# Optimization experiments

Hardware: AMD Instinct MI355X
Metric: run time of the kernel (lower is better)

The kernel has to match this reference:

```python
import jax, jax.numpy as jnp
import numpy as np

N = 5
RANK = 3
IMW = IMH = 1024
S = IMW * IMH
RANKLIST = [1] + [RANK] * (N - 1) + [1]  # [1,3,3,3,3,1]


def _xavier_std(shape):
    # torch xavier_normal_ on a 3D tensor (a, b, c): fan_in = b*c, fan_out = a*c
    a, b, c = shape
    fan_in, fan_out = b * c, a * c
    return float(np.sqrt(2.0 / (fan_in + fan_out)))


def setup_inputs() -> dict:
    key = jax.random.key(0)
    keys = jax.random.split(key, N + 1)
    inp = {"z": jax.random.normal(keys[0], (S,), dtype=jnp.float32)}
    for n in range(N):
        shp = (RANKLIST[n], S, RANKLIST[n + 1])
        inp[f"TT{n}"] = jax.random.normal(keys[n + 1], shp, dtype=jnp.float32) * _xavier_std(shp)
    return inp


def reference(z, TT0, TT1, TT2, TT3, TT4):
    # V[k] = z @ TT[k] : contract the s axis -> (r_k, r_{k+1}); tiny matrices.
    f = jnp.einsum('s,rsq->rq', z, TT0)          # (1, 3)
    for core in (TT1, TT2, TT3):
        f = f @ jnp.einsum('s,rsq->rq', z, core)  # (1, 3)
    # Last factor: the slice TT[N-1][:, :, 0] itself (NOT contracted with z).
    f = f @ TT4[:, :, 0]                          # (1, s)
    return f.reshape(-1)                          # (s,)
```

## Files before the change

kernel.cpp:

```cpp
#include <hip/hip_runtime.h>

#define SDIM (1024 * 1024)
#define GROUPS (SDIM / 4)
#define K1_BLOCKS 1024
#define K1_THREADS 256
#define NACC 30
#define PART_STRIDE 32

__device__ __forceinline__ float wave_reduce(float v) {
    #pragma unroll
    for (int off = 32; off > 0; off >>= 1)
        v += __shfl_down(v, off, 64);
    return v;
}

__global__ __launch_bounds__(K1_THREADS) void ftt_k1(
    const float* __restrict__ z,
    const float* __restrict__ t0,
    const float* __restrict__ t1,
    const float* __restrict__ t2,
    const float* __restrict__ t3,
    float* __restrict__ partials)
{
    float acc[NACC];
    #pragma unroll
    for (int i = 0; i < NACC; ++i) acc[i] = 0.0f;

    const int g = blockIdx.x * K1_THREADS + threadIdx.x;

    const float4 z4 = reinterpret_cast<const float4*>(z)[g];
    const float zz[4] = {z4.x, z4.y, z4.z, z4.w};

    {
        const float4* p = reinterpret_cast<const float4*>(t0 + 12 * g);
        const float4 c0 = p[0], c1 = p[1], c2 = p[2];
        const float tt[12] = {c0.x, c0.y, c0.z, c0.w,
                              c1.x, c1.y, c1.z, c1.w,
                              c2.x, c2.y, c2.z, c2.w};
        #pragma unroll
        for (int j = 0; j < 4; ++j)
            #pragma unroll
            for (int q = 0; q < 3; ++q)
                acc[q] += zz[j] * tt[j * 3 + q];
    }

    const float* __restrict__ Ts[3] = {t1, t2, t3};
    #pragma unroll
    for (int k = 0; k < 3; ++k) {
        #pragma unroll
        for (int r = 0; r < 3; ++r) {
            const float4* p = reinterpret_cast<const float4*>(Ts[k] + r * 3 * SDIM + 12 * g);
            const float4 c0 = p[0], c1 = p[1], c2 = p[2];
            const float tt[12] = {c0.x, c0.y, c0.z, c0.w,
                                  c1.x, c1.y, c1.z, c1.w,
                                  c2.x, c2.y, c2.z, c2.w};
            #pragma unroll
            for (int j = 0; j < 4; ++j)
                #pragma unroll
                for (int q = 0; q < 3; ++q)
                    acc[3 + k * 9 + r * 3 + q] += zz[j] * tt[j * 3 + q];
        }
    }

    #pragma unroll
    for (int i = 0; i < NACC; ++i)
        acc[i] = wave_reduce(acc[i]);

    __shared__ float red[4][NACC];
    const int lane = threadIdx.x & 63;
    const int wave = threadIdx.x >> 6;
    if (lane == 0) {
        #pragma unroll
        for (int i = 0; i < NACC; ++i) red[wave][i] = acc[i];
    }
    __syncthreads();
    if (threadIdx.x < NACC) {
        const float s = red[0][threadIdx.x] + red[1][threadIdx.x] +
                        red[2][threadIdx.x] + red[3][threadIdx.x];
        partials[blockIdx.x * PART_STRIDE + threadIdx.x] = s;
    }
}

__global__ __launch_bounds__(256) void ftt_k2(
    const float* __restrict__ partials,
    float* __restrict__ fvec)
{
    __shared__ float part[8][32];
    const int c = threadIdx.x & 31;
    const int grp = threadIdx.x >> 5;
    float s = 0.0f;
    const int b0 = grp * (K1_BLOCKS / 8);
    for (int b = b0; b < b0 + (K1_BLOCKS / 8); ++b)
        s += partials[b * PART_STRIDE + c];
    part[grp][c] = s;
    __syncthreads();

    if (threadIdx.x == 0) {
        float sum[NACC];
        #pragma unroll
        for (int i = 0; i < NACC; ++i) {
            float t = 0.0f;
            #pragma unroll
            for (int gg = 0; gg < 8; ++gg) t += part[gg][i];
            sum[i] = t;
        }
        float f0 = sum[0], f1 = sum[1], f2 = sum[2];
        #pragma unroll
        for (int k = 0; k < 3; ++k) {
            const float* V = &sum[3 + k * 9];
            const float n0 = f0 * V[0] + f1 * V[3] + f2 * V[6];
            const float n1 = f0 * V[1] + f1 * V[4] + f2 * V[7];
            const float n2 = f0 * V[2] + f1 * V[5] + f2 * V[8];
            f0 = n0; f1 = n1; f2 = n2;
        }
        fvec[0] = f0; fvec[1] = f1; fvec[2] = f2;
    }
}

__global__ __launch_bounds__(256) void ftt_k3(
    const float* __restrict__ t4,
    const float* __restrict__ fvec,
    float* __restrict__ out)
{
    const int i = blockIdx.x * blockDim.x + threadIdx.x;
    const float f0 = fvec[0], f1 = fvec[1], f2 = fvec[2];
    const float4 a = reinterpret_cast<const float4*>(t4)[i];
    const float4 b = reinterpret_cast<const float4*>(t4 + SDIM)[i];
    const float4 c = reinterpret_cast<const float4*>(t4 + 2 * SDIM)[i];
    float4 o;
    o.x = f0 * a.x + f1 * b.x + f2 * c.x;
    o.y = f0 * a.y + f1 * b.y + f2 * c.y;
    o.z = f0 * a.z + f1 * b.z + f2 * c.z;
    o.w = f0 * a.w + f1 * b.w + f2 * c.w;
    reinterpret_cast<float4*>(out)[i] = o;
}

extern "C" void kernel_launch(void* const* d_in, const int* in_sizes, int n_in,
                              void* d_out, int out_size, void* d_ws, size_t ws_size,
                              hipStream_t stream)
{
    const float* z  = (const float*)d_in[0];
    const float* t0 = (const float*)d_in[1];
    const float* t1 = (const float*)d_in[2];
    const float* t2 = (const float*)d_in[3];
    const float* t3 = (const float*)d_in[4];
    const float* t4 = (const float*)d_in[5];
    float* out = (float*)d_out;

    float* partials = (float*)d_ws;
    float* fvec     = partials + K1_BLOCKS * PART_STRIDE;

    ftt_k1<<<K1_BLOCKS, K1_THREADS, 0, stream>>>(z, t0, t1, t2, t3, partials);
    ftt_k2<<<1, 256, 0, stream>>>(partials, fvec);
    ftt_k3<<<SDIM / 4 / 256, 256, 0, stream>>>(t4, fvec, out);
}
```

Baseline: 172.3 us.

## Split TT-core contraction across a 2D grid of planes to cut register pressure

The first kernel now launches one grid row per (core, rank) plane, ten in total, and each thread contracts only 12 floats of one plane into 3 accumulators instead of 30. The goal is lower register usage, higher occupancy and more memory parallelism for the streaming read of about 120 MB. In exchange z is re-read once per plane, there are ten times as many blocks and partial sums, and the final reduction kernel is restructured to sum thirty partial columns.

```diff
diff --git a/kernel.cpp b/kernel.cpp
--- a/kernel.cpp
+++ b/kernel.cpp
@@ -2,19 +2,10 @@
 
 #define SDIM (1024 * 1024)
 #define GROUPS (SDIM / 4)
-#define K1_BLOCKS 1024
-#define K1_THREADS 256
-#define NACC 30
-#define PART_STRIDE 32
+#define CHUNKS 1024
+#define NPLANE 10
 
-__device__ __forceinline__ float wave_reduce(float v) {
-    #pragma unroll
-    for (int off = 32; off > 0; off >>= 1)
-        v += __shfl_down(v, off, 64);
-    return v;
-}
-
-__global__ __launch_bounds__(K1_THREADS) void ftt_k1(
+__global__ __launch_bounds__(256) void ftt_k1(
     const float* __restrict__ z,
     const float* __restrict__ t0,
     const float* __restrict__ t1,
@@ -22,62 +13,43 @@
     const float* __restrict__ t3,
     float* __restrict__ partials)
 {
-    float acc[NACC];
-    #pragma unroll
-    for (int i = 0; i < NACC; ++i) acc[i] = 0.0f;
+    const int plane = blockIdx.y;
+    const int g = blockIdx.x * 256 + threadIdx.x;
 
-    const int g = blockIdx.x * K1_THREADS + threadIdx.x;
+    const float* base;
+    if (plane == 0) {
+        base = t0;
+    } else {
+        const int pk = plane - 1;
+        const int k = pk / 3;
+        const float* tk = (k == 0) ? t1 : (k == 1) ? t2 : t3;
+        base = tk + (pk % 3) * (3 * SDIM);
+    }
 
     const float4 z4 = reinterpret_cast<const float4*>(z)[g];
-    const float zz[4] = {z4.x, z4.y, z4.z, z4.w};
+    const float4* p = reinterpret_cast<const float4*>(base + 12 * g);
+    const float4 c0 = p[0], c1 = p[1], c2 = p[2];
 
-    {
-        const float4* p = reinterpret_cast<const float4*>(t0 + 12 * g);
-        const float4 c0 = p[0], c1 = p[1], c2 = p[2];
-        const float tt[12] = {c0.x, c0.y, c0.z, c0.w,
-                              c1.x, c1.y, c1.z, c1.w,
-                              c2.x, c2.y, c2.z, c2.w};
-        #pragma unroll
-        for (int j = 0; j < 4; ++j)
-            #pragma unroll
-            for (int q = 0; q < 3; ++q)
-                acc[q] += zz[j] * tt[j * 3 + q];
+    float a0 = z4.x * c0.x + z4.y * c0.w + z4.z * c1.z + z4.w * c2.y;
+    float a1 = z4.x * c0.y + z4.y * c1.x + z4.z * c1.w + z4.w * c2.z;
+    float a2 = z4.x * c0.z + z4.y * c1.y + z4.z * c2.x + z4.w * c2.w;
+
+    #pragma unroll
+    for (int off = 32; off > 0; off >>= 1) {
+        a0 += __shfl_down(a0, off, 64);
+        a1 += __shfl_down(a1, off, 64);
+        a2 += __shfl_down(a2, off, 64);
     }
 
-    const float* __restrict__ Ts[3] = {t1, t2, t3};
-    #pragma unroll
-    for (int k = 0; k < 3; ++k) {
-        #pragma unroll
-        for (int r = 0; r < 3; ++r) {
-            const float4* p = reinterpret_cast<const float4*>(Ts[k] + r * 3 * SDIM + 12 * g);
-            const float4 c0 = p[0], c1 = p[1], c2 = p[2];
-            const float tt[12] = {c0.x, c0.y, c0.z, c0.w,
-                                  c1.x, c1.y, c1.z, c1.w,
-                                  c2.x, c2.y, c2.z, c2.w};
-            #pragma unroll
-            for (int j = 0; j < 4; ++j)
-                #pragma unroll
-                for (int q = 0; q < 3; ++q)
-                    acc[3 + k * 9 + r * 3 + q] += zz[j] * tt[j * 3 + q];
-        }
-    }
-
-    #pragma unroll
-    for (int i = 0; i < NACC; ++i)
-        acc[i] = wave_reduce(acc[i]);
-
-    __shared__ float red[4][NACC];
+    __shared__ float red[4][3];
     const int lane = threadIdx.x & 63;
     const int wave = threadIdx.x >> 6;
-    if (lane == 0) {
-        #pragma unroll
-        for (int i = 0; i < NACC; ++i) red[wave][i] = acc[i];
-    }
+    if (lane == 0) { red[wave][0] = a0; red[wave][1] = a1; red[wave][2] = a2; }
     __syncthreads();
-    if (threadIdx.x < NACC) {
-        const float s = red[0][threadIdx.x] + red[1][threadIdx.x] +
-                        red[2][threadIdx.x] + red[3][threadIdx.x];
-        partials[blockIdx.x * PART_STRIDE + threadIdx.x] = s;
+    if (threadIdx.x < 3) {
+        const int c = threadIdx.x;
+        const float s = red[0][c] + red[1][c] + red[2][c] + red[3][c];
+        partials[(plane * CHUNKS + blockIdx.x) * 4 + c] = s;
     }
 }
 
@@ -85,23 +57,27 @@
     const float* __restrict__ partials,
     float* __restrict__ fvec)
 {
-    __shared__ float part[8][32];
-    const int c = threadIdx.x & 31;
-    const int grp = threadIdx.x >> 5;
-    float s = 0.0f;
-    const int b0 = grp * (K1_BLOCKS / 8);
-    for (int b = b0; b < b0 + (K1_BLOCKS / 8); ++b)
-        s += partials[b * PART_STRIDE + c];
-    part[grp][c] = s;
+    __shared__ float red[NPLANE * 3][8];
+    const int job = threadIdx.x >> 3;
+    const int sub = threadIdx.x & 7;
+    if (job < NPLANE * 3) {
+        const int plane = job / 3, c = job % 3;
+        float s = 0.0f;
+        const int b0 = sub * (CHUNKS / 8);
+        #pragma unroll 4
+        for (int b = b0; b < b0 + (CHUNKS / 8); ++b)
+            s += partials[(plane * CHUNKS + b) * 4 + c];
+        red[job][sub] = s;
+    }
     __syncthreads();
 
     if (threadIdx.x == 0) {
-        float sum[NACC];
+        float sum[NPLANE * 3];
         #pragma unroll
-        for (int i = 0; i < NACC; ++i) {
+        for (int i = 0; i < NPLANE * 3; ++i) {
             float t = 0.0f;
             #pragma unroll
-            for (int gg = 0; gg < 8; ++gg) t += part[gg][i];
+            for (int g = 0; g < 8; ++g) t += red[i][g];
             sum[i] = t;
         }
         float f0 = sum[0], f1 = sum[1], f2 = sum[2];
@@ -148,9 +124,9 @@
     float* out = (float*)d_out;
 
     float* partials = (float*)d_ws;
-    float* fvec     = partials + K1_BLOCKS * PART_STRIDE;
+    float* fvec     = partials + NPLANE * CHUNKS * 4;
 
-    ftt_k1<<<K1_BLOCKS, K1_THREADS, 0, stream>>>(z, t0, t1, t2, t3, partials);
+    ftt_k1<<<dim3(CHUNKS, NPLANE), 256, 0, stream>>>(z, t0, t1, t2, t3, partials);
     ftt_k2<<<1, 256, 0, stream>>>(partials, fvec);
     ftt_k3<<<SDIM / 4 / 256, 256, 0, stream>>>(t4, fvec, out);
 }
```

Result: no change. 172.3 us (-0.0%).
